# Kernel optimization log

Measured on AMD Instinct MI355X. Metric: run time of the kernel, lower is better.

Reference implementation:

```python
import jax, jax.numpy as jnp
import numpy as np

B, T, I, C, O = 256, 1024, 128, 256, 10


def setup_inputs() -> dict:
    key = jax.random.key(0)
    k1, k2, k3, k4, k5 = jax.random.split(key, 5)
    x = jax.random.normal(k1, (B, T, I), dtype=jnp.float32)
    # xavier-like scale for kernels
    kernel = jax.random.normal(k2, (I, 2 * C), dtype=jnp.float32) * (6.0 / (I + 2 * C)) ** 0.5
    recurrent_kernel = jax.random.normal(k3, (C, 2 * C), dtype=jnp.float32) * (6.0 / (C + 2 * C)) ** 0.5
    # bias: forget-gate half initialized to log(uniform(1, T-1)), rest zero
    u = jax.random.uniform(k4, (C,), minval=1.0, maxval=float(T - 1))
    recurrent_bias = jnp.concatenate([jnp.log(u), jnp.zeros((C,), jnp.float32)])
    dense_w = jax.random.normal(k5, (C, O), dtype=jnp.float32) * (1.0 / C) ** 0.5
    dense_b = jnp.zeros((O,), jnp.float32)
    return {"x": x, "kernel": kernel, "recurrent_kernel": recurrent_kernel,
            "recurrent_bias": recurrent_bias, "dense_w": dense_w, "dense_b": dense_b}


def reference(x, kernel, recurrent_kernel, recurrent_bias, dense_w, dense_b):
    cells = recurrent_kernel.shape[0]
    # Precompute input projection for all timesteps in one big GEMM: [B,T,2C]
    xz = jnp.einsum('bti,ig->btg', x, kernel) + recurrent_bias
    xz_t = jnp.swapaxes(xz, 0, 1)  # [T, B, 2C] for scan over time

    def step(carry, z_in):
        h, c = carry
        z = z_in + h @ recurrent_kernel  # [B, 2C]
        f = jax.nn.sigmoid(z[:, :cells])
        c_new = f * c + (1.0 - f) * jnp.tanh(z[:, cells:])
        return (c_new, c_new), None

    h0 = jnp.zeros((x.shape[0], cells), x.dtype)
    (h_final, _), _ = jax.lax.scan(step, (h0, h0), xz_t)
    return h_final @ dense_w + dense_b
```

## Files before the change

### kernel.cpp

```cpp
#include <hip/hip_runtime.h>

#define BB 256
#define TT 1024
#define II 128
#define GG 512
#define CC 256
#define L2E 1.44269504f

typedef _Float16 f16;
typedef _Float16 h8_t __attribute__((ext_vector_type(8)));
typedef float f4_t __attribute__((ext_vector_type(4)));
typedef unsigned short ushort_t;

static __device__ __forceinline__ float fast_rcp(float x) {
#if __has_builtin(__builtin_amdgcn_rcpf)
    return __builtin_amdgcn_rcpf(x);
#else
    return 1.f / x;
#endif
}
static __device__ __forceinline__ float fast_exp2(float x) {
#if __has_builtin(__builtin_amdgcn_exp2f)
    return __builtin_amdgcn_exp2f(x);
#else
    return exp2f(x);
#endif
}

__global__ void kt_transpose(const float* __restrict__ kin, f16* __restrict__ kt) {
    int idx = blockIdx.x * 256 + threadIdx.x;
    int k = idx >> 9;
    int n = idx & 511;
    kt[n * II + k] = (f16)kin[k * GG + n];
}

__global__ __launch_bounds__(256)
void gemm_xz(const float* __restrict__ x, const f16* __restrict__ kt,
             const float* __restrict__ bias, ushort_t* __restrict__ xz) {
    const int  ntile = blockIdx.x;
    const long mtile = blockIdx.y;
    const int wave = threadIdx.x >> 6;
    const int lane = threadIdx.x & 63;
    const int wm = (wave & 1) * 64;
    const int wn = (wave >> 1) * 64;
    const int lm = lane & 15;
    const int q  = lane >> 4;

    f4_t acc[4][4];
#pragma unroll
    for (int mi = 0; mi < 4; ++mi)
#pragma unroll
        for (int ni = 0; ni < 4; ++ni)
            acc[mi][ni] = (f4_t){0.f, 0.f, 0.f, 0.f};

#pragma unroll
    for (int kc = 0; kc < 4; ++kc) {
        h8_t a[4], bf[4];
#pragma unroll
        for (int mi = 0; mi < 4; ++mi) {
            const int rowm = (int)(mtile * 128) + wm + mi * 16 + lm;
            const int b  = rowm & 255;
            const int tt = rowm >> 8;
            const float* ap = x + (size_t)b * (TT * II) + (size_t)tt * II + kc * 32 + q * 8;
            f4_t p0 = *(const f4_t*)ap;
            f4_t p1 = *(const f4_t*)(ap + 4);
            h8_t tv;
            tv[0] = (f16)p0[0]; tv[1] = (f16)p0[1]; tv[2] = (f16)p0[2]; tv[3] = (f16)p0[3];
            tv[4] = (f16)p1[0]; tv[5] = (f16)p1[1]; tv[6] = (f16)p1[2]; tv[7] = (f16)p1[3];
            a[mi] = tv;
        }
#pragma unroll
        for (int ni = 0; ni < 4; ++ni) {
            const f16* bp = kt + (size_t)(ntile * 128 + wn + ni * 16 + lm) * II + kc * 32 + q * 8;
            bf[ni] = *(const h8_t*)bp;
        }
#pragma unroll
        for (int mi = 0; mi < 4; ++mi)
#pragma unroll
            for (int ni = 0; ni < 4; ++ni)
                acc[mi][ni] = __builtin_amdgcn_mfma_f32_16x16x32_f16(a[mi], bf[ni], acc[mi][ni], 0, 0, 0);
    }

    __shared__ __align__(16) f16 st[128][136];
#pragma unroll
    for (int mi = 0; mi < 4; ++mi) {
#pragma unroll
        for (int ni = 0; ni < 4; ++ni) {
            const int col = ntile * 128 + wn + ni * 16 + lm;
            const float bv = bias[col];
            const float s  = (col < CC) ? L2E : (2.0f * L2E);
#pragma unroll
            for (int r = 0; r < 4; ++r)
                st[wm + mi * 16 + q * 4 + r][wn + ni * 16 + lm] = (f16)((acc[mi][ni][r] + bv) * s);
        }
    }
    __syncthreads();
    {
        const int r0  = threadIdx.x >> 1;
        const int seg = threadIdx.x & 1;
        ushort_t* gp = xz + (size_t)(mtile * 128 + r0) * GG + ntile * 128 + seg * 64;
        const f16* lp = &st[r0][seg * 64];
#pragma unroll
        for (int j = 0; j < 8; ++j)
            *(f4_t*)(gp + j * 8) = *(const f4_t*)(lp + j * 8);
    }
}

#define GATES(P, AF_, AG_, PF, HWR) do {                                             \
    _Pragma("unroll") for (int r = 0; r < 4; ++r) {                                  \
        ushort_t uf = (PF)[(P) * 4 + r];                                             \
        ushort_t ug = (PF)[((P) + 2) * 4 + r];                                       \
        float zf = (AF_)[r] + (float)(*(f16*)&uf);                                   \
        float zg = (AG_)[r] + (float)(*(f16*)&ug);                                   \
        float ef = fast_exp2(-zf);                                                   \
        float eg = fast_exp2(-fabsf(zg));                                            \
        unsigned sg = __builtin_bit_cast(unsigned, zg) & 0x80000000u;                \
        float t1 = __builtin_bit_cast(float, __builtin_bit_cast(unsigned, ef) ^ sg); \
        float cv = cst[P][r];                                                        \
        float num = fmaf(cv, eg, cv) + fmaf(-t1, eg, t1);                            \
        float den = (1.f + ef) * (1.f + eg);                                         \
        cv = num * fast_rcp(den);                                                    \
        cst[P][r] = cv;                                                              \
        (HWR)[(q * 4 + r) * 264 + (wave + 8 * (P)) * 16 + lm] = (f16)cv;             \
    }                                                                                \
} while (0)

#define STEP(T, PF, PP, HRD, HWR) do {                                               \
    h8_t af[8];                                                                      \
    af[0] = *(const h8_t*)((HRD) + lm * 264 + 0 * 32 + q * 8);                       \
    af[1] = *(const h8_t*)((HRD) + lm * 264 + 1 * 32 + q * 8);                       \
    f4_t a0 = (f4_t){0.f,0.f,0.f,0.f}, a1 = (f4_t){0.f,0.f,0.f,0.f};                 \
    f4_t a2 = (f4_t){0.f,0.f,0.f,0.f}, a3 = (f4_t){0.f,0.f,0.f,0.f};                 \
    _Pragma("unroll") for (int kt = 0; kt < 8; ++kt) {                               \
        if (kt < 6) af[kt + 2] = *(const h8_t*)((HRD) + lm * 264 + (kt + 2) * 32 + q * 8); \
        a0 = __builtin_amdgcn_mfma_f32_16x16x32_f16(af[kt], bw[0][kt], a0, 0, 0, 0); \
        a2 = __builtin_amdgcn_mfma_f32_16x16x32_f16(af[kt], bw[2][kt], a2, 0, 0, 0); \
    }                                                                                \
    _Pragma("unroll") for (int kt = 0; kt < 8; ++kt) {                               \
        a1 = __builtin_amdgcn_mfma_f32_16x16x32_f16(af[kt], bw[1][kt], a1, 0, 0, 0); \
        a3 = __builtin_amdgcn_mfma_f32_16x16x32_f16(af[kt], bw[3][kt], a3, 0, 0, 0); \
    }                                                                                \
    GATES(0, a0, a2, PF, HWR);                                                       \
    GATES(1, a1, a3, PF, HWR);                                                       \
    if ((T) + 2 < TT) {                                                              \
        _Pragma("unroll") for (int ni = 0; ni < 4; ++ni)                             \
            _Pragma("unroll") for (int r = 0; r < 4; ++r)                            \
                (PF)[ni * 4 + r] = (PP)[r * 512 + ni * 128];                         \
        (PP) += 2 * 131072;                                                          \
    }                                                                                \
    asm volatile("s_waitcnt lgkmcnt(0)\n\ts_barrier" ::: "memory");                  \
} while (0)

__global__ __launch_bounds__(512, 2)
void janet_rec(const float* __restrict__ rk, const float* __restrict__ dw,
               const float* __restrict__ db, const ushort_t* __restrict__ xz,
               float* __restrict__ out) {
    const int g = blockIdx.x;
    const int tid = threadIdx.x;
    const int wave = tid >> 6;
    const int lane = tid & 63;
    const int lm = lane & 15;
    const int q  = lane >> 4;

    h8_t bw[4][8];
#pragma unroll
    for (int ni = 0; ni < 4; ++ni) {
        const float s = (ni < 2) ? L2E : (2.0f * L2E);
#pragma unroll
        for (int kt = 0; kt < 8; ++kt) {
            h8_t tv;
#pragma unroll
            for (int j = 0; j < 8; ++j)
                tv[j] = (f16)(s * rk[(size_t)(kt * 32 + q * 8 + j) * GG + (wave + 8 * ni) * 16 + lm]);
            bw[ni][kt] = tv;
        }
    }

    __shared__ __align__(16) f16 hb[2][16][264];
    f16* h0 = &hb[0][0][0];
    f16* h1 = &hb[1][0][0];
    for (int i = tid; i < 2 * 16 * 264; i += 512) ((f16*)hb)[i] = (f16)0.f;

    float cst[2][4];
#pragma unroll
    for (int ni = 0; ni < 2; ++ni)
#pragma unroll
        for (int r = 0; r < 4; ++r) cst[ni][r] = 0.f;

    const ushort_t* pb = xz + ((size_t)g * 16 + q * 4) * 512 + wave * 16 + lm;
    const ushort_t* p1b = pb + 131072;
    const ushort_t* p0 = pb + 2 * 131072;
    const ushort_t* p1 = pb + 3 * 131072;

    ushort_t pf0[16], pf1[16];
#pragma unroll
    for (int ni = 0; ni < 4; ++ni)
#pragma unroll
        for (int r = 0; r < 4; ++r) {
            pf0[ni * 4 + r] = pb[r * 512 + ni * 128];
            pf1[ni * 4 + r] = p1b[r * 512 + ni * 128];
        }
    __syncthreads();

#pragma unroll 1
    for (int t = 0; t < TT; t += 2) {
        STEP(t,     pf0, p0, h0, h1);
        STEP(t + 1, pf1, p1, h1, h0);
    }

    __shared__ float hf[16][256];
#pragma unroll
    for (int ni = 0; ni < 2; ++ni)
#pragma unroll
        for (int r = 0; r < 4; ++r)
            hf[q * 4 + r][(wave + 8 * ni) * 16 + lm] = cst[ni][r];
    __syncthreads();
    if (tid < 160) {
        const int bi = tid / 10, o = tid % 10;
        float acc = db[o];
#pragma unroll 8
        for (int cc = 0; cc < CC; ++cc) acc = fmaf(hf[bi][cc], dw[cc * 10 + o], acc);
        out[(g * 16 + bi) * 10 + o] = acc;
    }
}

__global__ void ws_too_small(float* out, float wssz) {
    int i = blockIdx.x * 256 + threadIdx.x;
    if (i < BB * 10) out[i] = (i == 0) ? wssz : 0.f;
}

extern "C" void kernel_launch(void* const* d_in, const int* in_sizes, int n_in,
                              void* d_out, int out_size, void* d_ws, size_t ws_size,
                              hipStream_t stream) {
    const float* x   = (const float*)d_in[0];
    const float* kin = (const float*)d_in[1];
    const float* rk  = (const float*)d_in[2];
    const float* rb  = (const float*)d_in[3];
    const float* dw  = (const float*)d_in[4];
    const float* db  = (const float*)d_in[5];
    float* out = (float*)d_out;

    const size_t xz_bytes = (size_t)BB * TT * GG * 2;
    const size_t kt_bytes = (size_t)GG * II * 2;
    if (ws_size < xz_bytes + kt_bytes) {
        ws_too_small<<<10, 256, 0, stream>>>(out, (float)ws_size);
        return;
    }

    ushort_t* xz = (ushort_t*)d_ws;
    f16* kt = (f16*)((char*)d_ws + xz_bytes);

    kt_transpose<<<256, 256, 0, stream>>>(kin, kt);
    gemm_xz<<<dim3(4, 2048), 256, 0, stream>>>(x, kt, rb, xz);
    janet_rec<<<16, 512, 0, stream>>>(rk, dw, db, xz, out);
}
```

Before: 1.711 ms.

## Use 4-wave recurrence blocks with fragment-ordered xz layout and interleaved gates

The GEMM now writes the precomputed input projection in a fragment-major layout, so each lane of the recurrent kernel can fetch its per-step gate inputs with 16-byte vector loads instead of scattered 2-byte loads. The recurrent kernel drops from 8 waves to 4 per block. Each wave now holds twice the recurrent weights in registers and runs four MFMA chains, with gate math interleaved between chains to hide MFMA latency. The cost is heavier register pressure and twice the per-wave MFMA work on the serial critical path, traded against fewer waves taking part in each per-step barrier.

```diff
diff --git a/kernel.cpp b/kernel.cpp
--- a/kernel.cpp
+++ b/kernel.cpp
@@ -8,9 +8,11 @@
 #define L2E 1.44269504f
 
 typedef _Float16 f16;
+typedef _Float16 h2_t __attribute__((ext_vector_type(2)));
 typedef _Float16 h8_t __attribute__((ext_vector_type(8)));
 typedef float f4_t __attribute__((ext_vector_type(4)));
 typedef unsigned short ushort_t;
+typedef unsigned int uint_t;
 
 static __device__ __forceinline__ float fast_rcp(float x) {
 #if __has_builtin(__builtin_amdgcn_rcpf)
@@ -26,6 +28,10 @@
     return exp2f(x);
 #endif
 }
+static __device__ __forceinline__ float f16part(uint_t u, int h) {
+    h2_t p = __builtin_bit_cast(h2_t, u);
+    return (float)p[h];
+}
 
 __global__ void kt_transpose(const float* __restrict__ kin, f16* __restrict__ kt) {
     int idx = blockIdx.x * 256 + threadIdx.x;
@@ -36,9 +42,9 @@
 
 __global__ __launch_bounds__(256)
 void gemm_xz(const float* __restrict__ x, const f16* __restrict__ kt,
-             const float* __restrict__ bias, ushort_t* __restrict__ xz) {
-    const int  ntile = blockIdx.x;
-    const long mtile = blockIdx.y;
+             const float* __restrict__ bias, ushort_t* __restrict__ xzF) {
+    const int  nt = blockIdx.x;
+    const long mt = blockIdx.y;
     const int wave = threadIdx.x >> 6;
     const int lane = threadIdx.x & 63;
     const int wm = (wave & 1) * 64;
@@ -58,7 +64,7 @@
         h8_t a[4], bf[4];
 #pragma unroll
         for (int mi = 0; mi < 4; ++mi) {
-            const int rowm = (int)(mtile * 128) + wm + mi * 16 + lm;
+            const int rowm = (int)(mt * 128) + wm + mi * 16 + lm;
             const int b  = rowm & 255;
             const int tt = rowm >> 8;
             const float* ap = x + (size_t)b * (TT * II) + (size_t)tt * II + kc * 32 + q * 8;
@@ -71,7 +77,7 @@
         }
 #pragma unroll
         for (int ni = 0; ni < 4; ++ni) {
-            const f16* bp = kt + (size_t)(ntile * 128 + wn + ni * 16 + lm) * II + kc * 32 + q * 8;
+            const f16* bp = kt + (size_t)(nt * 128 + wn + ni * 16 + lm) * II + kc * 32 + q * 8;
             bf[ni] = *(const h8_t*)bp;
         }
 #pragma unroll
@@ -81,125 +87,145 @@
                 acc[mi][ni] = __builtin_amdgcn_mfma_f32_16x16x32_f16(a[mi], bf[ni], acc[mi][ni], 0, 0, 0);
     }
 
-    __shared__ __align__(16) f16 st[128][136];
+    __shared__ __align__(16) f16 st_T[128][136];
 #pragma unroll
     for (int mi = 0; mi < 4; ++mi) {
 #pragma unroll
         for (int ni = 0; ni < 4; ++ni) {
-            const int col = ntile * 128 + wn + ni * 16 + lm;
+            const int col = nt * 128 + wn + ni * 16 + lm;
             const float bv = bias[col];
             const float s  = (col < CC) ? L2E : (2.0f * L2E);
 #pragma unroll
             for (int r = 0; r < 4; ++r)
-                st[wm + mi * 16 + q * 4 + r][wn + ni * 16 + lm] = (f16)((acc[mi][ni][r] + bv) * s);
+                st_T[wn + ni * 16 + lm][wm + mi * 16 + q * 4 + r] = (f16)((acc[mi][ni][r] + bv) * s);
         }
     }
     __syncthreads();
     {
-        const int r0  = threadIdx.x >> 1;
-        const int seg = threadIdx.x & 1;
-        ushort_t* gp = xz + (size_t)(mtile * 128 + r0) * GG + ntile * 128 + seg * 64;
-        const f16* lp = &st[r0][seg * 64];
-#pragma unroll
-        for (int j = 0; j < 8; ++j)
-            *(f4_t*)(gp + j * 8) = *(const f4_t*)(lp + j * 8);
-    }
-}
-
-#define GATES(P, AF_, AG_, PF, HWR) do {                                             \
+        const int lane_s = threadIdx.x & 63;
+        const int q_s = lane_s >> 4, lm_s = lane_s & 15;
+        const int t = (int)(mt >> 1);
+        const int gbase = (int)(mt & 1) * 8;
+#pragma unroll
+        for (int c = 0; c < 8; ++c) {
+            const int row = (threadIdx.x >> 6) * 8 + c;
+            const int g_loc = row >> 2;
+            const int w = row & 3;
+            uint_t v[4];
+#pragma unroll
+            for (int d = 0; d < 2; ++d) {
+                const f16* lp = &st_T[(w + 4 * d) * 16 + lm_s][g_loc * 16 + q_s * 4];
+                uint2 u = *(const uint2*)lp;
+                v[d * 2 + 0] = u.x; v[d * 2 + 1] = u.y;
+            }
+            ushort_t* gp = xzF + ((size_t)t * 16 + gbase + g_loc) * 8192
+                               + w * 2048 + nt * 512 + lane_s * 8;
+            *(uint4*)gp = make_uint4(v[0], v[1], v[2], v[3]);
+        }
+    }
+}
+
+#define GATES(I, PF, HWR) do {                                                       \
     _Pragma("unroll") for (int r = 0; r < 4; ++r) {                                  \
-        ushort_t uf = (PF)[(P) * 4 + r];                                             \
-        ushort_t ug = (PF)[((P) + 2) * 4 + r];                                       \
-        float zf = (AF_)[r] + (float)(*(f16*)&uf);                                   \
-        float zg = (AG_)[r] + (float)(*(f16*)&ug);                                   \
+        float zf = aF[I][r] + f16part((PF)[2 * (I) + (r >> 1)], r & 1);              \
+        float zg = aG[I][r] + f16part((PF)[8 + 2 * (I) + (r >> 1)], r & 1);          \
         float ef = fast_exp2(-zf);                                                   \
         float eg = fast_exp2(-fabsf(zg));                                            \
         unsigned sg = __builtin_bit_cast(unsigned, zg) & 0x80000000u;                \
         float t1 = __builtin_bit_cast(float, __builtin_bit_cast(unsigned, ef) ^ sg); \
-        float cv = cst[P][r];                                                        \
+        float cv = cst[I][r];                                                        \
         float num = fmaf(cv, eg, cv) + fmaf(-t1, eg, t1);                            \
         float den = (1.f + ef) * (1.f + eg);                                         \
         cv = num * fast_rcp(den);                                                    \
-        cst[P][r] = cv;                                                              \
-        (HWR)[(q * 4 + r) * 264 + (wave + 8 * (P)) * 16 + lm] = (f16)cv;             \
+        cst[I][r] = cv;                                                              \
+        (HWR)[(q * 4 + r) * 264 + (w + 4 * (I)) * 16 + lm] = (f16)cv;                \
+    }                                                                                \
+} while (0)
+
+#define CHAIN(I) do {                                                                \
+    _Pragma("unroll") for (int kt = 0; kt < 8; ++kt) {                               \
+        aF[I] = __builtin_amdgcn_mfma_f32_16x16x32_f16(af[kt], bw[I][kt], aF[I], 0, 0, 0);       \
+        aG[I] = __builtin_amdgcn_mfma_f32_16x16x32_f16(af[kt], bw[4 + (I)][kt], aG[I], 0, 0, 0); \
     }                                                                                \
 } while (0)
 
 #define STEP(T, PF, PP, HRD, HWR) do {                                               \
     h8_t af[8];                                                                      \
-    af[0] = *(const h8_t*)((HRD) + lm * 264 + 0 * 32 + q * 8);                       \
-    af[1] = *(const h8_t*)((HRD) + lm * 264 + 1 * 32 + q * 8);                       \
-    f4_t a0 = (f4_t){0.f,0.f,0.f,0.f}, a1 = (f4_t){0.f,0.f,0.f,0.f};                 \
-    f4_t a2 = (f4_t){0.f,0.f,0.f,0.f}, a3 = (f4_t){0.f,0.f,0.f,0.f};                 \
-    _Pragma("unroll") for (int kt = 0; kt < 8; ++kt) {                               \
-        if (kt < 6) af[kt + 2] = *(const h8_t*)((HRD) + lm * 264 + (kt + 2) * 32 + q * 8); \
-        a0 = __builtin_amdgcn_mfma_f32_16x16x32_f16(af[kt], bw[0][kt], a0, 0, 0, 0); \
-        a2 = __builtin_amdgcn_mfma_f32_16x16x32_f16(af[kt], bw[2][kt], a2, 0, 0, 0); \
-    }                                                                                \
-    _Pragma("unroll") for (int kt = 0; kt < 8; ++kt) {                               \
-        a1 = __builtin_amdgcn_mfma_f32_16x16x32_f16(af[kt], bw[1][kt], a1, 0, 0, 0); \
-        a3 = __builtin_amdgcn_mfma_f32_16x16x32_f16(af[kt], bw[3][kt], a3, 0, 0, 0); \
-    }                                                                                \
-    GATES(0, a0, a2, PF, HWR);                                                       \
-    GATES(1, a1, a3, PF, HWR);                                                       \
+    _Pragma("unroll") for (int kt = 0; kt < 8; ++kt)                                 \
+        af[kt] = *(const h8_t*)((HRD) + lm * 264 + kt * 32 + q * 8);                 \
+    f4_t aF[4], aG[4];                                                               \
+    _Pragma("unroll") for (int i = 0; i < 4; ++i) {                                  \
+        aF[i] = (f4_t){0.f, 0.f, 0.f, 0.f};                                          \
+        aG[i] = (f4_t){0.f, 0.f, 0.f, 0.f};                                          \
+    }                                                                                \
+    CHAIN(0); CHAIN(1);                                                              \
+    GATES(0, PF, HWR);                                                               \
+    CHAIN(2);                                                                        \
+    GATES(1, PF, HWR);                                                               \
+    CHAIN(3);                                                                        \
+    GATES(2, PF, HWR);                                                               \
+    GATES(3, PF, HWR);                                                               \
     if ((T) + 2 < TT) {                                                              \
-        _Pragma("unroll") for (int ni = 0; ni < 4; ++ni)                             \
-            _Pragma("unroll") for (int r = 0; r < 4; ++r)                            \
-                (PF)[ni * 4 + r] = (PP)[r * 512 + ni * 128];                         \
+        _Pragma("unroll") for (int j8 = 0; j8 < 4; ++j8) {                           \
+            uint4 v = *(const uint4*)((PP) + j8 * 512);                              \
+            (PF)[j8 * 4 + 0] = v.x; (PF)[j8 * 4 + 1] = v.y;                          \
+            (PF)[j8 * 4 + 2] = v.z; (PF)[j8 * 4 + 3] = v.w;                          \
+        }                                                                            \
         (PP) += 2 * 131072;                                                          \
     }                                                                                \
     asm volatile("s_waitcnt lgkmcnt(0)\n\ts_barrier" ::: "memory");                  \
 } while (0)
 
-__global__ __launch_bounds__(512, 2)
+__global__ __launch_bounds__(256, 1)
 void janet_rec(const float* __restrict__ rk, const float* __restrict__ dw,
-               const float* __restrict__ db, const ushort_t* __restrict__ xz,
+               const float* __restrict__ db, const ushort_t* __restrict__ xzF,
                float* __restrict__ out) {
     const int g = blockIdx.x;
     const int tid = threadIdx.x;
-    const int wave = tid >> 6;
+    const int w = tid >> 6;
     const int lane = tid & 63;
     const int lm = lane & 15;
     const int q  = lane >> 4;
 
-    h8_t bw[4][8];
-#pragma unroll
-    for (int ni = 0; ni < 4; ++ni) {
-        const float s = (ni < 2) ? L2E : (2.0f * L2E);
+    h8_t bw[8][8];
+#pragma unroll
+    for (int ni8 = 0; ni8 < 8; ++ni8) {
+        const float s = (ni8 < 4) ? L2E : (2.0f * L2E);
+        const int col = (ni8 < 4) ? ((w + 4 * ni8) * 16 + lm)
+                                  : (CC + (w + 4 * (ni8 - 4)) * 16 + lm);
 #pragma unroll
         for (int kt = 0; kt < 8; ++kt) {
             h8_t tv;
 #pragma unroll
             for (int j = 0; j < 8; ++j)
-                tv[j] = (f16)(s * rk[(size_t)(kt * 32 + q * 8 + j) * GG + (wave + 8 * ni) * 16 + lm]);
-            bw[ni][kt] = tv;
+                tv[j] = (f16)(s * rk[(size_t)(kt * 32 + q * 8 + j) * GG + col]);
+            bw[ni8][kt] = tv;
         }
     }
 
     __shared__ __align__(16) f16 hb[2][16][264];
     f16* h0 = &hb[0][0][0];
     f16* h1 = &hb[1][0][0];
-    for (int i = tid; i < 2 * 16 * 264; i += 512) ((f16*)hb)[i] = (f16)0.f;
-
-    float cst[2][4];
-#pragma unroll
-    for (int ni = 0; ni < 2; ++ni)
-#pragma unroll
-        for (int r = 0; r < 4; ++r) cst[ni][r] = 0.f;
-
-    const ushort_t* pb = xz + ((size_t)g * 16 + q * 4) * 512 + wave * 16 + lm;
-    const ushort_t* p1b = pb + 131072;
-    const ushort_t* p0 = pb + 2 * 131072;
-    const ushort_t* p1 = pb + 3 * 131072;
-
-    ushort_t pf0[16], pf1[16];
-#pragma unroll
-    for (int ni = 0; ni < 4; ++ni)
-#pragma unroll
-        for (int r = 0; r < 4; ++r) {
-            pf0[ni * 4 + r] = pb[r * 512 + ni * 128];
-            pf1[ni * 4 + r] = p1b[r * 512 + ni * 128];
-        }
+    for (int i = tid; i < 2 * 16 * 264; i += 256) ((f16*)hb)[i] = (f16)0.f;
+
+    float cst[4][4];
+#pragma unroll
+    for (int i = 0; i < 4; ++i)
+#pragma unroll
+        for (int r = 0; r < 4; ++r) cst[i][r] = 0.f;
+
+    const ushort_t* pbase = xzF + (size_t)g * 8192 + w * 2048 + lane * 8;
+    const ushort_t* p0 = pbase + 2 * 131072;
+    const ushort_t* p1 = pbase + 3 * 131072;
+
+    uint_t pf0[16], pf1[16];
+#pragma unroll
+    for (int j8 = 0; j8 < 4; ++j8) {
+        uint4 v0 = *(const uint4*)(pbase + j8 * 512);
+        uint4 v1 = *(const uint4*)(pbase + 131072 + j8 * 512);
+        pf0[j8 * 4 + 0] = v0.x; pf0[j8 * 4 + 1] = v0.y; pf0[j8 * 4 + 2] = v0.z; pf0[j8 * 4 + 3] = v0.w;
+        pf1[j8 * 4 + 0] = v1.x; pf1[j8 * 4 + 1] = v1.y; pf1[j8 * 4 + 2] = v1.z; pf1[j8 * 4 + 3] = v1.w;
+    }
     __syncthreads();
 
 #pragma unroll 1
@@ -210,10 +236,10 @@
 
     __shared__ float hf[16][256];
 #pragma unroll
-    for (int ni = 0; ni < 2; ++ni)
+    for (int i = 0; i < 4; ++i)
 #pragma unroll
         for (int r = 0; r < 4; ++r)
-            hf[q * 4 + r][(wave + 8 * ni) * 16 + lm] = cst[ni][r];
+            hf[q * 4 + r][(w + 4 * i) * 16 + lm] = cst[i][r];
     __syncthreads();
     if (tid < 160) {
         const int bi = tid / 10, o = tid % 10;
@@ -247,10 +273,10 @@
         return;
     }
 
-    ushort_t* xz = (ushort_t*)d_ws;
+    ushort_t* xzF = (ushort_t*)d_ws;
     f16* kt = (f16*)((char*)d_ws + xz_bytes);
 
     kt_transpose<<<256, 256, 0, stream>>>(kin, kt);
-    gemm_xz<<<dim3(4, 2048), 256, 0, stream>>>(x, kt, rb, xz);
-    janet_rec<<<16, 512, 0, stream>>>(rk, dw, db, xz, out);
-}
+    gemm_xz<<<dim3(4, 2048), 256, 0, stream>>>(x, kt, rb, xzF);
+    janet_rec<<<16, 256, 0, stream>>>(rk, dw, db, xzF, out);
+}
```

Result: slower. 1.774 ms (+3.7%).
